# Kernel tuning notes

Measured on AMD Instinct MI355X. Metric: run time of the kernel, lower is better.

Reference implementation:

```python
import jax, jax.numpy as jnp
import numpy as np


def setup_inputs() -> dict:
    key = jax.random.key(0)
    k1, k2, k3 = jax.random.split(key, 3)
    B, S, D = 4, 2048, 1024
    x = jax.random.normal(k1, (B, S, D), dtype=jnp.float32)
    w_qkv = jax.random.normal(k2, (D, 3 * D), dtype=jnp.float32) * (D ** -0.5)
    b_qkv = jnp.zeros((3 * D,), dtype=jnp.float32)
    w_proj = jax.random.normal(k3, (D, D), dtype=jnp.float32) * (D ** -0.5)
    b_proj = jnp.zeros((D,), dtype=jnp.float32)
    return {"x": x, "w_qkv": w_qkv, "b_qkv": b_qkv, "w_proj": w_proj, "b_proj": b_proj}


def reference(x, w_qkv, b_qkv, w_proj, b_proj):
    B, S, D = x.shape
    H = 16
    hd = D // H
    scale = hd ** -0.5
    qkv = x @ w_qkv + b_qkv  # [B,S,3D]
    q, k, v = jnp.split(qkv, 3, axis=-1)
    # [B,S,D] -> [B,H,S,hd]
    q = q.reshape(B, S, H, hd).transpose(0, 2, 1, 3)
    k = k.reshape(B, S, H, hd).transpose(0, 2, 1, 3)
    v = v.reshape(B, S, H, hd).transpose(0, 2, 1, 3)
    attn = jnp.einsum('bhqd,bhkd->bhqk', q, k) * scale
    attn = jax.nn.softmax(attn, axis=-1)
    out = jnp.einsum('bhqk,bhkd->bhqd', attn, v)  # [B,H,S,hd]
    out = out.transpose(0, 2, 1, 3).reshape(B, S, D)
    return out @ w_proj + b_proj
```

## Files before the change

kernel.cpp:

```cpp
#include <hip/hip_runtime.h>
#include <stdint.h>

typedef __bf16 bf16x8 __attribute__((ext_vector_type(8)));
typedef float f32x4 __attribute__((ext_vector_type(4)));
typedef float f32x16 __attribute__((ext_vector_type(16)));
typedef unsigned short u16x8 __attribute__((ext_vector_type(8)));

__device__ __forceinline__ unsigned short f2bf(float f) {
  union { float f; uint32_t u; } v; v.f = f;
  uint32_t r = v.u + 0x7FFFu + ((v.u >> 16) & 1u);
  return (unsigned short)(r >> 16);
}

__device__ __forceinline__ f32x4 mfma16(bf16x8 a, bf16x8 b, f32x4 c) {
  return __builtin_amdgcn_mfma_f32_16x16x32_bf16(a, b, c, 0, 0, 0);
}

__device__ __forceinline__ f32x16 mfma32(bf16x8 a, bf16x8 b, f32x16 c) {
  return __builtin_amdgcn_mfma_f32_32x32x16_bf16(a, b, c, 0, 0, 0);
}

__device__ __forceinline__ uint32_t cvtpk(float lo, float hi) {
  uint32_t r;
  asm("v_cvt_pk_bf16_f32 %0, %1, %2" : "=v"(r) : "v"(lo), "v"(hi));
  return r;
}

__device__ __forceinline__ void gload_lds16(const unsigned short* g, unsigned short* l) {
  __builtin_amdgcn_global_load_lds(
      (const __attribute__((address_space(1))) void*)g,
      (__attribute__((address_space(3))) void*)l, 16, 0, 0);
}

#define SCALEQ 0.18033688011112042f
#define FIXSHIFT 12.0f

__global__ __launch_bounds__(256) void convert_f32_bf16(const float* __restrict__ in,
                                                        unsigned short* __restrict__ outp) {
  int i = blockIdx.x * 256 + threadIdx.x;
  const float4* p = (const float4*)in + (size_t)i * 2;
  float4 a = p[0], b = p[1];
  u16x8 o;
  o[0] = f2bf(a.x); o[1] = f2bf(a.y); o[2] = f2bf(a.z); o[3] = f2bf(a.w);
  o[4] = f2bf(b.x); o[5] = f2bf(b.y); o[6] = f2bf(b.z); o[7] = f2bf(b.w);
  *(u16x8*)&outp[(size_t)i * 8] = o;
}

__global__ __launch_bounds__(256) void transpose_to_bf16(const float* __restrict__ w,
                                                         unsigned short* __restrict__ wT,
                                                         int K, int N) {
  __shared__ unsigned short tile[64][72];
  const int n0 = blockIdx.x * 64, k0 = blockIdx.y * 64;
  const int t = threadIdx.x;
  {
    const int r = t >> 4, c0 = (t & 15) * 4;
#pragma unroll
    for (int i = 0; i < 4; ++i) {
      int rr = r + i * 16;
      float4 v = *(const float4*)&w[(size_t)(k0 + rr) * N + n0 + c0];
      tile[c0 + 0][rr] = f2bf(v.x);
      tile[c0 + 1][rr] = f2bf(v.y);
      tile[c0 + 2][rr] = f2bf(v.z);
      tile[c0 + 3][rr] = f2bf(v.w);
    }
  }
  __syncthreads();
  {
    const int c = t >> 2, r0 = (t & 3) * 16;
    u16x8 o1, o2;
#pragma unroll
    for (int i = 0; i < 8; ++i) { o1[i] = tile[c][r0 + i]; o2[i] = tile[c][r0 + 8 + i]; }
    *(u16x8*)&wT[(size_t)(n0 + c) * K + k0 + r0] = o1;
    *(u16x8*)&wT[(size_t)(n0 + c) * K + k0 + r0 + 8] = o2;
  }
}

__global__ __launch_bounds__(256) void qkv_gemm(const unsigned short* __restrict__ xbf,
                                                const unsigned short* __restrict__ wT,
                                                const float* __restrict__ bias,
                                                unsigned short* __restrict__ qb,
                                                unsigned short* __restrict__ kb,
                                                unsigned short* __restrict__ vf) {
  __shared__ unsigned short As[128 * 32];
  __shared__ unsigned short Bs[128 * 32];
  const int tid = threadIdx.x, lane = tid & 63, wave = tid >> 6;
  const int mb = blockIdx.y * 128, nb = blockIdx.x * 128;
  const int wr = (wave >> 1) * 64, wc = (wave & 1) * 64;
  const int fr = lane & 15, fk = (lane >> 4) * 8;
  f32x4 acc[4][4] = {};
  for (int kt = 0; kt < 1024; kt += 32) {
    __syncthreads();
#pragma unroll
    for (int i = 0; i < 2; ++i) {
      int ch = wave * 128 + i * 64 + lane;
      int r = ch >> 2, ko = (ch & 3) * 8;
      gload_lds16(xbf + (size_t)(mb + r) * 1024 + kt + ko, &As[(wave * 128 + i * 64) * 8]);
      gload_lds16(wT + (size_t)(nb + r) * 1024 + kt + ko, &Bs[(wave * 128 + i * 64) * 8]);
    }
    __syncthreads();
    bf16x8 a[4], bq[4];
#pragma unroll
    for (int m = 0; m < 4; ++m) a[m] = *(const bf16x8*)&As[(wr + m * 16 + fr) * 32 + fk];
#pragma unroll
    for (int n = 0; n < 4; ++n) bq[n] = *(const bf16x8*)&Bs[(wc + n * 16 + fr) * 32 + fk];
#pragma unroll
    for (int m = 0; m < 4; ++m)
#pragma unroll
      for (int n = 0; n < 4; ++n) acc[m][n] = mfma16(a[m], bq[n], acc[m][n]);
  }
#pragma unroll
  for (int m = 0; m < 4; ++m)
#pragma unroll
    for (int n = 0; n < 4; ++n) {
      int col = nb + wc + n * 16 + fr;
      float bv = bias[col];
      int type = col >> 10, cc = col & 1023, h = cc >> 6, d = cc & 63;
#pragma unroll
      for (int j4 = 0; j4 < 4; ++j4) {
        int row = mb + wr + m * 16 + (lane >> 4) * 4 + j4;
        int bidx = row >> 11, s = row & 2047;
        int bh = bidx * 16 + h;
        float val = acc[m][n][j4] + bv;
        if (type == 0) {
          qb[(((size_t)bh) * 2048 + s) * 64 + d] = f2bf(val * SCALEQ);
        } else if (type == 1) {
          kb[(((size_t)bh) * 2048 + s) * 64 + d] = f2bf(val);
        } else {
          int t = s >> 5;
          int u = ((d >> 5) << 1) + ((s >> 4) & 1);
          int l = (((s >> 2) & 1) << 5) + (d & 31);
          int jj = (s & 3) + (((s >> 3) & 1) << 2);
          size_t idx = ((((size_t)bh * 64 + t) * 4 + u) * 64 + l) * 8 + jj;
          vf[idx] = f2bf(val);
        }
      }
    }
}

__global__ __launch_bounds__(256, 2) void attn_kernel(const unsigned short* __restrict__ qg,
                                                      const unsigned short* __restrict__ kgl,
                                                      const unsigned short* __restrict__ vf,
                                                      unsigned short* __restrict__ attnb) {
  const int tid = threadIdx.x;
  const int lane = tid & 63, wave = tid >> 6;
  const int l31 = lane & 31, hl = lane >> 5;
  const int h8 = hl * 8;

  const int L = blockIdx.y * 8 + blockIdx.x;
  const int xcd = L & 7, sl = L >> 3;
  const int bh = xcd * 8 + (sl & 7);
  const int qt = sl >> 3;
  const int b = bh >> 4, hh = bh & 15;

  const unsigned short* Qg = qg + (size_t)bh * 2048 * 64;
  const unsigned short* Kg = kgl + (size_t)bh * 2048 * 64;
  const unsigned short* VfB = vf + (size_t)bh * 131072 + lane * 8;
  const int q0 = qt * 256 + wave * 64;

  bf16x8 qf[2][4];
#pragma unroll
  for (int s2 = 0; s2 < 2; ++s2)
#pragma unroll
    for (int dw = 0; dw < 4; ++dw)
      qf[s2][dw] = *(const bf16x8*)&Qg[(size_t)(q0 + s2 * 32 + l31) * 64 + dw * 16 + h8];

  f32x16 o[2][2] = {};
  f32x4 lacc[2] = {};

  f32x16 cinit;
#pragma unroll
  for (int r = 0; r < 16; ++r) cinit[r] = -FIXSHIFT;

  union PU { uint32_t u[4]; bf16x8 v; };

  bf16x8 ka0, ka1, ka2, ka3, va0, va1, va2, va3;
  bf16x8 kb0, kb1, kb2, kb3, vb0, vb1, vb2, vb3;
  {
    const unsigned short* kr = &Kg[(size_t)l31 * 64 + h8];
    ka0 = *(const bf16x8*)&kr[0];
    ka1 = *(const bf16x8*)&kr[16];
    ka2 = *(const bf16x8*)&kr[32];
    ka3 = *(const bf16x8*)&kr[48];
    va0 = *(const bf16x8*)&VfB[0];
    va1 = *(const bf16x8*)&VfB[512];
    va2 = *(const bf16x8*)&VfB[1024];
    va3 = *(const bf16x8*)&VfB[1536];
  }

#define STEP(K0, K1, K2, K3, V0, V1, V2, V3)                                  \
  {                                                                           \
    _Pragma("unroll")                                                         \
    for (int s2 = 0; s2 < 2; ++s2) {                                          \
      f32x16 sa = mfma32(K0, qf[s2][0], cinit);                               \
      sa = mfma32(K1, qf[s2][1], sa);                                         \
      sa = mfma32(K2, qf[s2][2], sa);                                         \
      sa = mfma32(K3, qf[s2][3], sa);                                         \
      _Pragma("unroll")                                                       \
      for (int r = 0; r < 16; ++r) sa[r] = __builtin_amdgcn_exp2f(sa[r]);     \
      _Pragma("unroll")                                                       \
      for (int j = 0; j < 4; ++j)                                             \
        lacc[s2][j] += (sa[j] + sa[4 + j]) + (sa[8 + j] + sa[12 + j]);        \
      PU p0, p1;                                                              \
      p0.u[0] = cvtpk(sa[0], sa[1]);   p0.u[1] = cvtpk(sa[2], sa[3]);         \
      p0.u[2] = cvtpk(sa[4], sa[5]);   p0.u[3] = cvtpk(sa[6], sa[7]);         \
      p1.u[0] = cvtpk(sa[8], sa[9]);   p1.u[1] = cvtpk(sa[10], sa[11]);       \
      p1.u[2] = cvtpk(sa[12], sa[13]); p1.u[3] = cvtpk(sa[14], sa[15]);       \
      o[s2][0] = mfma32(V0, p0.v, o[s2][0]);                                  \
      o[s2][0] = mfma32(V1, p1.v, o[s2][0]);                                  \
      o[s2][1] = mfma32(V2, p0.v, o[s2][1]);                                  \
      o[s2][1] = mfma32(V3, p1.v, o[s2][1]);                                  \
    }                                                                         \
  }

  for (int t = 0; t < 64; t += 2) {
    {
      const unsigned short* kr = &Kg[(size_t)((t + 1) * 32 + l31) * 64 + h8];
      const unsigned short* vp = VfB + (size_t)(t + 1) * 2048;
      kb0 = *(const bf16x8*)&kr[0];
      kb1 = *(const bf16x8*)&kr[16];
      kb2 = *(const bf16x8*)&kr[32];
      kb3 = *(const bf16x8*)&kr[48];
      vb0 = *(const bf16x8*)&vp[0];
      vb1 = *(const bf16x8*)&vp[512];
      vb2 = *(const bf16x8*)&vp[1024];
      vb3 = *(const bf16x8*)&vp[1536];
    }
    STEP(ka0, ka1, ka2, ka3, va0, va1, va2, va3);
    if (t + 2 < 64) {
      const unsigned short* kr = &Kg[(size_t)((t + 2) * 32 + l31) * 64 + h8];
      const unsigned short* vp = VfB + (size_t)(t + 2) * 2048;
      ka0 = *(const bf16x8*)&kr[0];
      ka1 = *(const bf16x8*)&kr[16];
      ka2 = *(const bf16x8*)&kr[32];
      ka3 = *(const bf16x8*)&kr[48];
      va0 = *(const bf16x8*)&vp[0];
      va1 = *(const bf16x8*)&vp[512];
      va2 = *(const bf16x8*)&vp[1024];
      va3 = *(const bf16x8*)&vp[1536];
    }
    STEP(kb0, kb1, kb2, kb3, vb0, vb1, vb2, vb3);
  }
#undef STEP

#pragma unroll
  for (int s2 = 0; s2 < 2; ++s2) {
    float l = (lacc[s2][0] + lacc[s2][1]) + (lacc[s2][2] + lacc[s2][3]);
    l += __shfl_xor(l, 32);
    float invl = 1.0f / l;
    const size_t base = ((size_t)(b * 2048 + q0 + s2 * 32 + l31)) * 1024 + hh * 64;
#pragma unroll
    for (int r = 0; r < 16; ++r) {
      int d = (r & 3) + 8 * (r >> 2) + 4 * hl;
      attnb[base + d] = f2bf(o[s2][0][r] * invl);
      attnb[base + 32 + d] = f2bf(o[s2][1][r] * invl);
    }
  }
}

__global__ __launch_bounds__(256) void proj_gemm(const unsigned short* __restrict__ abf,
                                                 const unsigned short* __restrict__ wT,
                                                 const float* __restrict__ bias,
                                                 float* __restrict__ outp) {
  __shared__ unsigned short As[128 * 32];
  __shared__ unsigned short Bs[128 * 32];
  const int tid = threadIdx.x, lane = tid & 63, wave = tid >> 6;
  const int mb = blockIdx.y * 128, nb = blockIdx.x * 128;
  const int wr = (wave >> 1) * 64, wc = (wave & 1) * 64;
  const int fr = lane & 15, fk = (lane >> 4) * 8;
  f32x4 acc[4][4] = {};
  for (int kt = 0; kt < 1024; kt += 32) {
    __syncthreads();
#pragma unroll
    for (int i = 0; i < 2; ++i) {
      int ch = wave * 128 + i * 64 + lane;
      int r = ch >> 2, ko = (ch & 3) * 8;
      gload_lds16(abf + (size_t)(mb + r) * 1024 + kt + ko, &As[(wave * 128 + i * 64) * 8]);
      gload_lds16(wT + (size_t)(nb + r) * 1024 + kt + ko, &Bs[(wave * 128 + i * 64) * 8]);
    }
    __syncthreads();
    bf16x8 a[4], bq[4];
#pragma unroll
    for (int m = 0; m < 4; ++m) a[m] = *(const bf16x8*)&As[(wr + m * 16 + fr) * 32 + fk];
#pragma unroll
    for (int n = 0; n < 4; ++n) bq[n] = *(const bf16x8*)&Bs[(wc + n * 16 + fr) * 32 + fk];
#pragma unroll
    for (int m = 0; m < 4; ++m)
#pragma unroll
      for (int n = 0; n < 4; ++n) acc[m][n] = mfma16(a[m], bq[n], acc[m][n]);
  }
#pragma unroll
  for (int m = 0; m < 4; ++m)
#pragma unroll
    for (int n = 0; n < 4; ++n) {
      int col = nb + wc + n * 16 + fr;
      float bv = bias[col];
#pragma unroll
      for (int j = 0; j < 4; ++j) {
        int row = mb + wr + m * 16 + (lane >> 4) * 4 + j;
        outp[(size_t)row * 1024 + col] = acc[m][n][j] + bv;
      }
    }
}

extern "C" void kernel_launch(void* const* d_in, const int* in_sizes, int n_in,
                              void* d_out, int out_size, void* d_ws, size_t ws_size,
                              hipStream_t stream) {
  const float* x = (const float*)d_in[0];
  const float* w_qkv = (const float*)d_in[1];
  const float* b_qkv = (const float*)d_in[2];
  const float* w_proj = (const float*)d_in[3];
  const float* b_proj = (const float*)d_in[4];
  float* outp = (float*)d_out;
  char* ws = (char*)d_ws;

  const size_t OFF_XBF = 0;
  const size_t OFF_WTQKV = 16777216;
  const size_t OFF_WTPROJ = 23068672;
  const size_t OFF_Q = 25165824;
  const size_t OFF_K = 41943040;
  const size_t OFF_VF = 58720256;
  const size_t NEED = 75497472;
  if (ws_size < NEED) return;

  unsigned short* xbf = (unsigned short*)(ws + OFF_XBF);
  unsigned short* wTqkv = (unsigned short*)(ws + OFF_WTQKV);
  unsigned short* wTproj = (unsigned short*)(ws + OFF_WTPROJ);
  unsigned short* qbuf = (unsigned short*)(ws + OFF_Q);
  unsigned short* kbuf = (unsigned short*)(ws + OFF_K);
  unsigned short* vfbuf = (unsigned short*)(ws + OFF_VF);
  unsigned short* attnb = xbf;

  hipLaunchKernelGGL(convert_f32_bf16, dim3(4096), dim3(256), 0, stream, x, xbf);
  hipLaunchKernelGGL(transpose_to_bf16, dim3(48, 16), dim3(256), 0, stream, w_qkv, wTqkv, 1024, 3072);
  hipLaunchKernelGGL(transpose_to_bf16, dim3(16, 16), dim3(256), 0, stream, w_proj, wTproj, 1024, 1024);
  hipLaunchKernelGGL(qkv_gemm, dim3(24, 64), dim3(256), 0, stream, xbf, wTqkv, b_qkv, qbuf, kbuf, vfbuf);
  hipLaunchKernelGGL(attn_kernel, dim3(8, 64), dim3(256), 0, stream, qbuf, kbuf, vfbuf, attnb);
  hipLaunchKernelGGL(proj_gemm, dim3(8, 64), dim3(256), 0, stream, attnb, wTproj, b_proj, outp);
}
```

Before: 209.5 us.

## Vectorize V and attention-output stores, add per-iteration barrier in attention loop

The QKV epilogue now writes the V fragment layout as one packed 4-element bf16 store instead of four scalar stores, exploiting the fact that the four rows map to consecutive jj slots. The attention output epilogue packs four bf16 values per 8-byte store. A workgroup barrier is inserted at the top of each K/V iteration, apparently to keep waves in lockstep so they share cache lines for K/V loads. The barrier adds sync overhead and may reduce latency hiding between waves.

```diff
diff --git a/kernel.cpp b/kernel.cpp
--- a/kernel.cpp
+++ b/kernel.cpp
@@ -5,6 +5,7 @@
 typedef float f32x4 __attribute__((ext_vector_type(4)));
 typedef float f32x16 __attribute__((ext_vector_type(16)));
 typedef unsigned short u16x8 __attribute__((ext_vector_type(8)));
+typedef unsigned short u16x4 __attribute__((ext_vector_type(4)));
 
 __device__ __forceinline__ unsigned short f2bf(float f) {
   union { float f; uint32_t u; } v; v.f = f;
@@ -115,24 +116,26 @@
       int col = nb + wc + n * 16 + fr;
       float bv = bias[col];
       int type = col >> 10, cc = col & 1023, h = cc >> 6, d = cc & 63;
-#pragma unroll
-      for (int j4 = 0; j4 < 4; ++j4) {
-        int row = mb + wr + m * 16 + (lane >> 4) * 4 + j4;
-        int bidx = row >> 11, s = row & 2047;
-        int bh = bidx * 16 + h;
-        float val = acc[m][n][j4] + bv;
-        if (type == 0) {
-          qb[(((size_t)bh) * 2048 + s) * 64 + d] = f2bf(val * SCALEQ);
-        } else if (type == 1) {
-          kb[(((size_t)bh) * 2048 + s) * 64 + d] = f2bf(val);
-        } else {
-          int t = s >> 5;
-          int u = ((d >> 5) << 1) + ((s >> 4) & 1);
-          int l = (((s >> 2) & 1) << 5) + (d & 31);
-          int jj = (s & 3) + (((s >> 3) & 1) << 2);
-          size_t idx = ((((size_t)bh * 64 + t) * 4 + u) * 64 + l) * 8 + jj;
-          vf[idx] = f2bf(val);
-        }
+      int row0 = mb + wr + m * 16 + (lane >> 4) * 4;
+      int bidx = row0 >> 11, s0 = row0 & 2047;
+      int bh = bidx * 16 + h;
+      if (type == 0) {
+#pragma unroll
+        for (int j4 = 0; j4 < 4; ++j4)
+          qb[((size_t)bh * 2048 + s0 + j4) * 64 + d] = f2bf((acc[m][n][j4] + bv) * SCALEQ);
+      } else if (type == 1) {
+#pragma unroll
+        for (int j4 = 0; j4 < 4; ++j4)
+          kb[((size_t)bh * 2048 + s0 + j4) * 64 + d] = f2bf(acc[m][n][j4] + bv);
+      } else {
+        int t = s0 >> 5;
+        int u = ((d >> 5) << 1) + ((s0 >> 4) & 1);
+        int l = (((s0 >> 2) & 1) << 5) + (d & 31);
+        int jj0 = ((s0 >> 3) & 1) << 2;
+        u16x4 pk;
+#pragma unroll
+        for (int j4 = 0; j4 < 4; ++j4) pk[j4] = f2bf(acc[m][n][j4] + bv);
+        *(u16x4*)&vf[((((size_t)bh * 64 + t) * 4 + u) * 64 + l) * 8 + jj0] = pk;
       }
     }
 }
@@ -213,6 +216,7 @@
   }
 
   for (int t = 0; t < 64; t += 2) {
+    __builtin_amdgcn_s_barrier();
     {
       const unsigned short* kr = &Kg[(size_t)((t + 1) * 32 + l31) * 64 + h8];
       const unsigned short* vp = VfB + (size_t)(t + 1) * 2048;
@@ -249,10 +253,16 @@
     float invl = 1.0f / l;
     const size_t base = ((size_t)(b * 2048 + q0 + s2 * 32 + l31)) * 1024 + hh * 64;
 #pragma unroll
-    for (int r = 0; r < 16; ++r) {
-      int d = (r & 3) + 8 * (r >> 2) + 4 * hl;
-      attnb[base + d] = f2bf(o[s2][0][r] * invl);
-      attnb[base + 32 + d] = f2bf(o[s2][1][r] * invl);
+    for (int g = 0; g < 4; ++g) {
+      u16x4 w0, w1;
+#pragma unroll
+      for (int j = 0; j < 4; ++j) {
+        w0[j] = f2bf(o[s2][0][g * 4 + j] * invl);
+        w1[j] = f2bf(o[s2][1][g * 4 + j] * invl);
+      }
+      int d = 8 * g + 4 * hl;
+      *(u16x4*)&attnb[base + d] = w0;
+      *(u16x4*)&attnb[base + 32 + d] = w1;
     }
   }
 }
```

Result: slower. 226.2 us (+8.0%).
